# Optimization experiments

Measured on AMD Instinct MI355X. Metric: run time of the kernel, lower is better.

The kernel has to match this reference:

```python
import jax, jax.numpy as jnp
import numpy as np

B = 128
T = 784
H = 256
N_CLASSES = 10


def setup_inputs() -> dict:
    key = jax.random.key(0)
    ks = jax.random.split(key, 7)
    s = 1.0 / np.sqrt(H)
    inputs = jax.random.normal(ks[0], (B, T), dtype=jnp.float32)
    # fixed permutation, matching np.random.RandomState(92916).permutation(784)
    perm = jnp.asarray(np.random.RandomState(92916).permutation(T), dtype=jnp.int32)
    W_ih = jax.random.uniform(ks[1], (4 * H, 1), jnp.float32, -s, s)
    W_hh = jax.random.uniform(ks[2], (4 * H, H), jnp.float32, -s, s)
    b_ih = jax.random.uniform(ks[3], (4 * H,), jnp.float32, -s, s)
    b_hh = jax.random.uniform(ks[4], (4 * H,), jnp.float32, -s, s)
    lin_W = jax.random.uniform(ks[5], (N_CLASSES, H), jnp.float32, -s, s)
    lin_b = jax.random.uniform(ks[6], (N_CLASSES,), jnp.float32, -s, s)
    return {"inputs": inputs, "perm": perm, "W_ih": W_ih, "W_hh": W_hh,
            "b_ih": b_ih, "b_hh": b_hh, "lin_W": lin_W, "lin_b": lin_b}


def reference(inputs, perm, W_ih, W_hh, b_ih, b_hh, lin_W, lin_b):
    # permuted sequential MNIST
    x = inputs[:, perm]                      # [B, T]
    b = b_ih + b_hh                          # [4H]
    w_in = W_ih[:, 0]                        # [4H], input size is 1

    def step(carry, x_t):
        h, c = carry                         # each [B, H]
        gates = x_t[:, None] * w_in[None, :] + h @ W_hh.T + b  # [B, 4H]
        i, f, g, o = jnp.split(gates, 4, axis=-1)
        i = jax.nn.sigmoid(i)
        f = jax.nn.sigmoid(f)
        g = jnp.tanh(g)
        o = jax.nn.sigmoid(o)
        c = f * c + i * g
        h = o * jnp.tanh(c)
        return (h, c), None

    h0 = jnp.zeros((x.shape[0], W_hh.shape[1]), dtype=x.dtype)
    (h, c), _ = jax.lax.scan(step, (h0, h0), x.T)  # scan over T, xs [T, B]
    return h @ lin_W.T + lin_b               # [B, n_classes]
```

## Files before the change

kernel.cpp:

```cpp
#include <hip/hip_runtime.h>

#define TSTEPS 784
#define BATCH  128
#define HID    256
#define WPG    8
#define BG     4
#define NGRP   (BATCH / BG)
#define COLS   32
#define RLOC   128
typedef unsigned long long u64;

__global__ void prep_x(const float* __restrict__ in, const int* __restrict__ perm,
                       float* __restrict__ xp) {
    int b = blockIdx.x;
    for (int t = threadIdx.x; t < TSTEPS; t += blockDim.x)
        xp[b * TSTEPS + t] = in[b * TSTEPS + perm[t]];
}

__global__ void prep_slots(u64* __restrict__ slots) {
    int i = blockIdx.x * blockDim.x + threadIdx.x;
    if (i < BATCH * HID)          slots[i] = 0ull;
    else if (i < 2 * BATCH * HID) slots[i] = 0xFFFFFFFF00000000ull;
}

__global__ __launch_bounds__(1024, 4) void lstm_kernel(
    const float* __restrict__ Whh, const float* __restrict__ Wih,
    const float* __restrict__ bih, const float* __restrict__ bhh,
    const float* __restrict__ xp, u64* __restrict__ slots)
{
    __shared__ float h_lds[BG * HID];
    __shared__ float gate_lds[BG * 132];
    __shared__ float x_lds[BG * TSTEPS];
    __shared__ float c_lds[BG * COLS];
    __shared__ float bias_lds[RLOC];
    __shared__ float win_lds[RLOC];

    const int tid = threadIdx.x;
    const int g       = blockIdx.x & 31;
    const int wgi     = blockIdx.x >> 5;
    const int B0      = g * BG;
    const int colbase = wgi * COLS;

    const int r = tid >> 3;
    const int s = tid & 7;
    const int gate = r >> 5;
    const int R = gate * 256 + colbase + (r & 31);

    float4 w0, w1, w2, w3, w4, w5, w6, w7;
    {
        const float4* wp = (const float4*)(Whh + R * HID + s * 32);
        w0 = wp[(0 + s) & 7]; w1 = wp[(1 + s) & 7];
        w2 = wp[(2 + s) & 7]; w3 = wp[(3 + s) & 7];
        w4 = wp[(4 + s) & 7]; w5 = wp[(5 + s) & 7];
        w6 = wp[(6 + s) & 7]; w7 = wp[(7 + s) & 7];
    }
    #define KEEP4(V) asm volatile("" : "+v"((V).x), "+v"((V).y), "+v"((V).z), "+v"((V).w))
    KEEP4(w0); KEEP4(w1); KEEP4(w2); KEEP4(w3);
    KEEP4(w4); KEEP4(w5); KEEP4(w6); KEEP4(w7);
    #undef KEEP4

    if (tid < RLOC) {
        int gr = (tid >> 5) * 256 + colbase + (tid & 31);
        bias_lds[tid] = bih[gr] + bhh[gr];
        win_lds[tid]  = Wih[gr];
    }
    #pragma unroll
    for (int b = 0; b < BG; ++b)
        if (tid < TSTEPS) x_lds[b * TSTEPS + tid] = xp[(B0 + b) * TSTEPS + tid];
    if (tid < BG * COLS) c_lds[tid] = 0.f;
    __syncthreads();

    const int pb = tid >> 8, pk = tid & 255;
    u64* const slot0 = slots + (B0 + pb) * HID + pk;
    u64* const slot1 = slots + BATCH * HID + (B0 + pb) * HID + pk;

    for (int t = 0; t < TSTEPS; ++t) {
        {
            u64* sp = (t & 1) ? slot1 : slot0;
            u64 v;
            do {
                v = __hip_atomic_load(sp, __ATOMIC_RELAXED, __HIP_MEMORY_SCOPE_AGENT);
            } while ((unsigned)(v >> 32) != (unsigned)t);
            h_lds[tid] = __uint_as_float((unsigned)v);
        }
        __syncthreads();

        float a0 = 0.f, a1 = 0.f, a2 = 0.f, a3 = 0.f;
        const float* hbase = h_lds + s * 32;
        #define DOT_STEP(d, wd)                                              \
        {                                                                    \
            int off = (((d) + s) & 7) * 4;                                   \
            float4 hq0 = *(const float4*)(hbase + off);                      \
            float4 hq1 = *(const float4*)(hbase + 256 + off);                \
            float4 hq2 = *(const float4*)(hbase + 512 + off);                \
            float4 hq3 = *(const float4*)(hbase + 768 + off);                \
            a0 = fmaf(wd.x, hq0.x, a0); a0 = fmaf(wd.y, hq0.y, a0);          \
            a0 = fmaf(wd.z, hq0.z, a0); a0 = fmaf(wd.w, hq0.w, a0);          \
            a1 = fmaf(wd.x, hq1.x, a1); a1 = fmaf(wd.y, hq1.y, a1);          \
            a1 = fmaf(wd.z, hq1.z, a1); a1 = fmaf(wd.w, hq1.w, a1);          \
            a2 = fmaf(wd.x, hq2.x, a2); a2 = fmaf(wd.y, hq2.y, a2);          \
            a2 = fmaf(wd.z, hq2.z, a2); a2 = fmaf(wd.w, hq2.w, a2);          \
            a3 = fmaf(wd.x, hq3.x, a3); a3 = fmaf(wd.y, hq3.y, a3);          \
            a3 = fmaf(wd.z, hq3.z, a3); a3 = fmaf(wd.w, hq3.w, a3);          \
        }
        DOT_STEP(0, w0) DOT_STEP(1, w1) DOT_STEP(2, w2) DOT_STEP(3, w3)
        DOT_STEP(4, w4) DOT_STEP(5, w5) DOT_STEP(6, w6) DOT_STEP(7, w7)
        #undef DOT_STEP

        #pragma unroll
        for (int m = 1; m < 8; m <<= 1) {
            a0 += __shfl_xor(a0, m, 64);
            a1 += __shfl_xor(a1, m, 64);
            a2 += __shfl_xor(a2, m, 64);
            a3 += __shfl_xor(a3, m, 64);
        }
        if (s < BG) {
            float sum = (s == 0) ? a0 : (s == 1) ? a1 : (s == 2) ? a2 : a3;
            float xv = x_lds[s * TSTEPS + t];
            float full = fmaf(win_lds[r], xv, sum + bias_lds[r]);
            float act;
            if (gate == 2) act = 2.f / (1.f + __expf(-2.f * full)) - 1.f;
            else           act = 1.f / (1.f + __expf(-full));
            gate_lds[s * 132 + r] = act;
        }
        __syncthreads();

        if (tid < BG * COLS) {
            int b = tid >> 5, j = tid & 31;
            float iv = gate_lds[b * 132 + j];
            float fv = gate_lds[b * 132 + 32 + j];
            float gv = gate_lds[b * 132 + 64 + j];
            float ov = gate_lds[b * 132 + 96 + j];
            float cn = fmaf(fv, c_lds[tid], iv * gv);
            c_lds[tid] = cn;
            float tc = 2.f / (1.f + __expf(-2.f * cn)) - 1.f;
            float hn = ov * tc;
            u64 val = ((u64)(unsigned)(t + 1) << 32) | (u64)__float_as_uint(hn);
            u64* dp = slots + ((t + 1) & 1) * (BATCH * HID)
                            + (B0 + b) * HID + colbase + j;
            __hip_atomic_store(dp, val, __ATOMIC_RELAXED, __HIP_MEMORY_SCOPE_AGENT);
        }
    }
}

__global__ void out_kernel(const u64* __restrict__ slots, const float* __restrict__ linW,
                           const float* __restrict__ linb, float* __restrict__ out) {
    __shared__ float hl[HID];
    int b = blockIdx.x;
    for (int k = threadIdx.x; k < HID; k += blockDim.x)
        hl[k] = __uint_as_float((unsigned)slots[b * HID + k]);
    __syncthreads();
    if (threadIdx.x < 10) {
        int n = threadIdx.x;
        float acc = linb[n];
        for (int k = 0; k < HID; ++k) acc = fmaf(hl[k], linW[n * HID + k], acc);
        out[b * 10 + n] = acc;
    }
}

extern "C" void kernel_launch(void* const* d_in, const int* in_sizes, int n_in,
                              void* d_out, int out_size, void* d_ws, size_t ws_size,
                              hipStream_t stream) {
    const float* inputs = (const float*)d_in[0];
    const int*   perm   = (const int*)d_in[1];
    const float* Wih    = (const float*)d_in[2];
    const float* Whh    = (const float*)d_in[3];
    const float* bih    = (const float*)d_in[4];
    const float* bhh    = (const float*)d_in[5];
    const float* linW   = (const float*)d_in[6];
    const float* linb   = (const float*)d_in[7];
    float* out = (float*)d_out;

    u64*   slots = (u64*)d_ws;
    float* xp    = (float*)(slots + 2 * BATCH * HID);

    prep_x<<<BATCH, 256, 0, stream>>>(inputs, perm, xp);
    prep_slots<<<(2 * BATCH * HID + 255) / 256, 256, 0, stream>>>(slots);
    lstm_kernel<<<NGRP * WPG, 1024, 0, stream>>>(Whh, Wih, bih, bhh, xp, slots);
    out_kernel<<<BATCH, 64, 0, stream>>>(slots, linW, linb, out);
}
```

Baseline: 2.244 ms.

## Restructure LSTM step so each lane owns all four gates, dropping gate LDS barrier

Each 16-lane group now holds the weights of all four gates for one hidden column and computes two batch rows, so the whole cell update (gates, c, h) is done in registers and the gate_lds staging and second __syncthreads per step go away. The dot products use packed v_pk_fma_f32 and the cross-lane reduction uses DPP adds instead of shfl_xor. h is double-buffered in padded LDS, which makes one barrier per step enough. The trade-off is redundant activation math across the 16 lanes and hand-written inline asm whose correctness depends on DPP row semantics.

```diff
diff --git a/kernel.cpp b/kernel.cpp
--- a/kernel.cpp
+++ b/kernel.cpp
@@ -7,8 +7,11 @@
 #define BG     4
 #define NGRP   (BATCH / BG)
 #define COLS   32
-#define RLOC   128
+#define KSTR   68
+#define HBUF   (16 * KSTR)
 typedef unsigned long long u64;
+typedef float v4f __attribute__((ext_vector_type(4)));
+typedef float v2f __attribute__((ext_vector_type(2)));
 
 __global__ void prep_x(const float* __restrict__ in, const int* __restrict__ perm,
                        float* __restrict__ xp) {
@@ -23,17 +26,22 @@
     else if (i < 2 * BATCH * HID) slots[i] = 0xFFFFFFFF00000000ull;
 }
 
+#define PK_FMA(acc, a, b) \
+    asm("v_pk_fma_f32 %0, %1, %2, %0" : "+v"(acc) : "v"(a), "v"(b))
+#define DPP_ADD(x, ctl) asm("v_add_f32 %0, %1, %0 " ctl " row_mask:0xf bank_mask:0xf" \
+                            : "+v"(x) : "v"(x))
+#define LO2(V) __builtin_shufflevector(V, V, 0, 1)
+#define HI2(V) __builtin_shufflevector(V, V, 2, 3)
+
 __global__ __launch_bounds__(1024, 4) void lstm_kernel(
     const float* __restrict__ Whh, const float* __restrict__ Wih,
     const float* __restrict__ bih, const float* __restrict__ bhh,
     const float* __restrict__ xp, u64* __restrict__ slots)
 {
-    __shared__ float h_lds[BG * HID];
-    __shared__ float gate_lds[BG * 132];
+    __shared__ float h_lds[2][HBUF];
     __shared__ float x_lds[BG * TSTEPS];
-    __shared__ float c_lds[BG * COLS];
-    __shared__ float bias_lds[RLOC];
-    __shared__ float win_lds[RLOC];
+    __shared__ v4f   bias4[COLS];
+    __shared__ v4f   win4[COLS];
 
     const int tid = threadIdx.x;
     const int g       = blockIdx.x & 31;
@@ -41,104 +49,155 @@
     const int B0      = g * BG;
     const int colbase = wgi * COLS;
 
-    const int r = tid >> 3;
-    const int s = tid & 7;
-    const int gate = r >> 5;
-    const int R = gate * 256 + colbase + (r & 31);
-
-    float4 w0, w1, w2, w3, w4, w5, w6, w7;
-    {
-        const float4* wp = (const float4*)(Whh + R * HID + s * 32);
-        w0 = wp[(0 + s) & 7]; w1 = wp[(1 + s) & 7];
-        w2 = wp[(2 + s) & 7]; w3 = wp[(3 + s) & 7];
-        w4 = wp[(4 + s) & 7]; w5 = wp[(5 + s) & 7];
-        w6 = wp[(6 + s) & 7]; w7 = wp[(7 + s) & 7];
-    }
-    #define KEEP4(V) asm volatile("" : "+v"((V).x), "+v"((V).y), "+v"((V).z), "+v"((V).w))
-    KEEP4(w0); KEEP4(w1); KEEP4(w2); KEEP4(w3);
-    KEEP4(w4); KEEP4(w5); KEEP4(w6); KEEP4(w7);
-    #undef KEEP4
-
-    if (tid < RLOC) {
-        int gr = (tid >> 5) * 256 + colbase + (tid & 31);
-        bias_lds[tid] = bih[gr] + bhh[gr];
-        win_lds[tid]  = Wih[gr];
-    }
+    const int ks  = tid & 15;
+    const int bp  = (tid >> 4) & 1;
+    const int col = tid >> 5;
+
+    v4f w[4][4];
     #pragma unroll
-    for (int b = 0; b < BG; ++b)
-        if (tid < TSTEPS) x_lds[b * TSTEPS + tid] = xp[(B0 + b) * TSTEPS + tid];
-    if (tid < BG * COLS) c_lds[tid] = 0.f;
+    for (int q = 0; q < 4; ++q) {
+        const v4f* wp = (const v4f*)(Whh + (q * 256 + colbase + col) * HID + 16 * ks);
+        w[q][0] = wp[0]; w[q][1] = wp[1]; w[q][2] = wp[2]; w[q][3] = wp[3];
+    }
+    if (tid < COLS) {
+        v4f b4, w4_;
+        #pragma unroll
+        for (int q = 0; q < 4; ++q) {
+            int R = q * 256 + colbase + tid;
+            b4[q] = bih[R] + bhh[R];
+            w4_[q] = Wih[R];
+        }
+        bias4[tid] = b4; win4[tid] = w4_;
+    }
+    #pragma unroll
+    for (int bb = 0; bb < BG; ++bb)
+        if (tid < TSTEPS) x_lds[bb * TSTEPS + tid] = xp[(B0 + bb) * TSTEPS + tid];
     __syncthreads();
 
     const int pb = tid >> 8, pk = tid & 255;
     u64* const slot0 = slots + (B0 + pb) * HID + pk;
     u64* const slot1 = slots + BATCH * HID + (B0 + pb) * HID + pk;
+    const int hidx = (pk >> 4) * KSTR + pb * 16 + (pk & 15);
+
+    float c0 = 0.f, c1 = 0.f;
 
     for (int t = 0; t < TSTEPS; ++t) {
-        {
-            u64* sp = (t & 1) ? slot1 : slot0;
+        const int cur = t & 1;
+        #pragma unroll
+        for (int q = 0; q < 4; ++q)
+            asm volatile("" : "+v"(w[q][0]), "+v"(w[q][1]), "+v"(w[q][2]), "+v"(w[q][3]));
+
+        {
+            u64* sp = cur ? slot1 : slot0;
             u64 v;
-            do {
-                v = __hip_atomic_load(sp, __ATOMIC_RELAXED, __HIP_MEMORY_SCOPE_AGENT);
+            do { v = __hip_atomic_load(sp, __ATOMIC_RELAXED, __HIP_MEMORY_SCOPE_AGENT);
             } while ((unsigned)(v >> 32) != (unsigned)t);
-            h_lds[tid] = __uint_as_float((unsigned)v);
+            h_lds[cur][hidx] = __uint_as_float((unsigned)v);
         }
         __syncthreads();
 
-        float a0 = 0.f, a1 = 0.f, a2 = 0.f, a3 = 0.f;
-        const float* hbase = h_lds + s * 32;
-        #define DOT_STEP(d, wd)                                              \
-        {                                                                    \
-            int off = (((d) + s) & 7) * 4;                                   \
-            float4 hq0 = *(const float4*)(hbase + off);                      \
-            float4 hq1 = *(const float4*)(hbase + 256 + off);                \
-            float4 hq2 = *(const float4*)(hbase + 512 + off);                \
-            float4 hq3 = *(const float4*)(hbase + 768 + off);                \
-            a0 = fmaf(wd.x, hq0.x, a0); a0 = fmaf(wd.y, hq0.y, a0);          \
-            a0 = fmaf(wd.z, hq0.z, a0); a0 = fmaf(wd.w, hq0.w, a0);          \
-            a1 = fmaf(wd.x, hq1.x, a1); a1 = fmaf(wd.y, hq1.y, a1);          \
-            a1 = fmaf(wd.z, hq1.z, a1); a1 = fmaf(wd.w, hq1.w, a1);          \
-            a2 = fmaf(wd.x, hq2.x, a2); a2 = fmaf(wd.y, hq2.y, a2);          \
-            a2 = fmaf(wd.z, hq2.z, a2); a2 = fmaf(wd.w, hq2.w, a2);          \
-            a3 = fmaf(wd.x, hq3.x, a3); a3 = fmaf(wd.y, hq3.y, a3);          \
-            a3 = fmaf(wd.z, hq3.z, a3); a3 = fmaf(wd.w, hq3.w, a3);          \
-        }
-        DOT_STEP(0, w0) DOT_STEP(1, w1) DOT_STEP(2, w2) DOT_STEP(3, w3)
-        DOT_STEP(4, w4) DOT_STEP(5, w5) DOT_STEP(6, w6) DOT_STEP(7, w7)
-        #undef DOT_STEP
-
-        #pragma unroll
-        for (int m = 1; m < 8; m <<= 1) {
-            a0 += __shfl_xor(a0, m, 64);
-            a1 += __shfl_xor(a1, m, 64);
-            a2 += __shfl_xor(a2, m, 64);
-            a3 += __shfl_xor(a3, m, 64);
-        }
-        if (s < BG) {
-            float sum = (s == 0) ? a0 : (s == 1) ? a1 : (s == 2) ? a2 : a3;
-            float xv = x_lds[s * TSTEPS + t];
-            float full = fmaf(win_lds[r], xv, sum + bias_lds[r]);
-            float act;
-            if (gate == 2) act = 2.f / (1.f + __expf(-2.f * full)) - 1.f;
-            else           act = 1.f / (1.f + __expf(-full));
-            gate_lds[s * 132 + r] = act;
-        }
-        __syncthreads();
-
-        if (tid < BG * COLS) {
-            int b = tid >> 5, j = tid & 31;
-            float iv = gate_lds[b * 132 + j];
-            float fv = gate_lds[b * 132 + 32 + j];
-            float gv = gate_lds[b * 132 + 64 + j];
-            float ov = gate_lds[b * 132 + 96 + j];
-            float cn = fmaf(fv, c_lds[tid], iv * gv);
-            c_lds[tid] = cn;
-            float tc = 2.f / (1.f + __expf(-2.f * cn)) - 1.f;
-            float hn = ov * tc;
-            u64 val = ((u64)(unsigned)(t + 1) << 32) | (u64)__float_as_uint(hn);
-            u64* dp = slots + ((t + 1) & 1) * (BATCH * HID)
-                            + (B0 + b) * HID + colbase + j;
-            __hip_atomic_store(dp, val, __ATOMIC_RELAXED, __HIP_MEMORY_SCOPE_AGENT);
+        const float* hb = &h_lds[cur][ks * KSTR + bp * 32];
+        v2f a00 = {0.f,0.f}, a10 = {0.f,0.f}, a20 = {0.f,0.f}, a30 = {0.f,0.f};
+        v2f a01 = {0.f,0.f}, a11 = {0.f,0.f}, a21 = {0.f,0.f}, a31 = {0.f,0.f};
+        {
+            v4f hc0 = *(const v4f*)(hb + 0);
+            v4f hc1 = *(const v4f*)(hb + 4);
+            v4f hc2 = *(const v4f*)(hb + 8);
+            v4f hc3 = *(const v4f*)(hb + 12);
+            PK_FMA(a00, LO2(w[0][0]), LO2(hc0)); PK_FMA(a00, HI2(w[0][0]), HI2(hc0));
+            PK_FMA(a00, LO2(w[0][1]), LO2(hc1)); PK_FMA(a00, HI2(w[0][1]), HI2(hc1));
+            PK_FMA(a00, LO2(w[0][2]), LO2(hc2)); PK_FMA(a00, HI2(w[0][2]), HI2(hc2));
+            PK_FMA(a00, LO2(w[0][3]), LO2(hc3)); PK_FMA(a00, HI2(w[0][3]), HI2(hc3));
+            PK_FMA(a10, LO2(w[1][0]), LO2(hc0)); PK_FMA(a10, HI2(w[1][0]), HI2(hc0));
+            PK_FMA(a10, LO2(w[1][1]), LO2(hc1)); PK_FMA(a10, HI2(w[1][1]), HI2(hc1));
+            PK_FMA(a10, LO2(w[1][2]), LO2(hc2)); PK_FMA(a10, HI2(w[1][2]), HI2(hc2));
+            PK_FMA(a10, LO2(w[1][3]), LO2(hc3)); PK_FMA(a10, HI2(w[1][3]), HI2(hc3));
+            PK_FMA(a20, LO2(w[2][0]), LO2(hc0)); PK_FMA(a20, HI2(w[2][0]), HI2(hc0));
+            PK_FMA(a20, LO2(w[2][1]), LO2(hc1)); PK_FMA(a20, HI2(w[2][1]), HI2(hc1));
+            PK_FMA(a20, LO2(w[2][2]), LO2(hc2)); PK_FMA(a20, HI2(w[2][2]), HI2(hc2));
+            PK_FMA(a20, LO2(w[2][3]), LO2(hc3)); PK_FMA(a20, HI2(w[2][3]), HI2(hc3));
+            PK_FMA(a30, LO2(w[3][0]), LO2(hc0)); PK_FMA(a30, HI2(w[3][0]), HI2(hc0));
+            PK_FMA(a30, LO2(w[3][1]), LO2(hc1)); PK_FMA(a30, HI2(w[3][1]), HI2(hc1));
+            PK_FMA(a30, LO2(w[3][2]), LO2(hc2)); PK_FMA(a30, HI2(w[3][2]), HI2(hc2));
+            PK_FMA(a30, LO2(w[3][3]), LO2(hc3)); PK_FMA(a30, HI2(w[3][3]), HI2(hc3));
+        }
+        {
+            v4f hc0 = *(const v4f*)(hb + 16);
+            v4f hc1 = *(const v4f*)(hb + 20);
+            v4f hc2 = *(const v4f*)(hb + 24);
+            v4f hc3 = *(const v4f*)(hb + 28);
+            PK_FMA(a01, LO2(w[0][0]), LO2(hc0)); PK_FMA(a01, HI2(w[0][0]), HI2(hc0));
+            PK_FMA(a01, LO2(w[0][1]), LO2(hc1)); PK_FMA(a01, HI2(w[0][1]), HI2(hc1));
+            PK_FMA(a01, LO2(w[0][2]), LO2(hc2)); PK_FMA(a01, HI2(w[0][2]), HI2(hc2));
+            PK_FMA(a01, LO2(w[0][3]), LO2(hc3)); PK_FMA(a01, HI2(w[0][3]), HI2(hc3));
+            PK_FMA(a11, LO2(w[1][0]), LO2(hc0)); PK_FMA(a11, HI2(w[1][0]), HI2(hc0));
+            PK_FMA(a11, LO2(w[1][1]), LO2(hc1)); PK_FMA(a11, HI2(w[1][1]), HI2(hc1));
+            PK_FMA(a11, LO2(w[1][2]), LO2(hc2)); PK_FMA(a11, HI2(w[1][2]), HI2(hc2));
+            PK_FMA(a11, LO2(w[1][3]), LO2(hc3)); PK_FMA(a11, HI2(w[1][3]), HI2(hc3));
+            PK_FMA(a21, LO2(w[2][0]), LO2(hc0)); PK_FMA(a21, HI2(w[2][0]), HI2(hc0));
+            PK_FMA(a21, LO2(w[2][1]), LO2(hc1)); PK_FMA(a21, HI2(w[2][1]), HI2(hc1));
+            PK_FMA(a21, LO2(w[2][2]), LO2(hc2)); PK_FMA(a21, HI2(w[2][2]), HI2(hc2));
+            PK_FMA(a21, LO2(w[2][3]), LO2(hc3)); PK_FMA(a21, HI2(w[2][3]), HI2(hc3));
+            PK_FMA(a31, LO2(w[3][0]), LO2(hc0)); PK_FMA(a31, HI2(w[3][0]), HI2(hc0));
+            PK_FMA(a31, LO2(w[3][1]), LO2(hc1)); PK_FMA(a31, HI2(w[3][1]), HI2(hc1));
+            PK_FMA(a31, LO2(w[3][2]), LO2(hc2)); PK_FMA(a31, HI2(w[3][2]), HI2(hc2));
+            PK_FMA(a31, LO2(w[3][3]), LO2(hc3)); PK_FMA(a31, HI2(w[3][3]), HI2(hc3));
+        }
+        float s00 = a00.x + a00.y, s10 = a10.x + a10.y;
+        float s20 = a20.x + a20.y, s30 = a30.x + a30.y;
+        float s01 = a01.x + a01.y, s11 = a11.x + a11.y;
+        float s21 = a21.x + a21.y, s31 = a31.x + a31.y;
+
+        #define RSTAGE(ctl) \
+            DPP_ADD(s00, ctl); DPP_ADD(s10, ctl); DPP_ADD(s20, ctl); DPP_ADD(s30, ctl); \
+            DPP_ADD(s01, ctl); DPP_ADD(s11, ctl); DPP_ADD(s21, ctl); DPP_ADD(s31, ctl);
+        RSTAGE("quad_perm:[1,0,3,2]")
+        RSTAGE("quad_perm:[2,3,0,1]")
+        RSTAGE("row_half_mirror")
+        RSTAGE("row_mirror")
+        #undef RSTAGE
+
+        v4f b4 = bias4[col];
+        v4f wn = win4[col];
+        {
+            float xv = x_lds[(2 * bp) * TSTEPS + t];
+            float p0 = fmaf(wn.x, xv, s00 + b4.x);
+            float p1 = fmaf(wn.y, xv, s10 + b4.y);
+            float p2 = fmaf(wn.z, xv, s20 + b4.z);
+            float p3 = fmaf(wn.w, xv, s30 + b4.w);
+            float iv = 1.f / (1.f + __expf(-p0));
+            float fv = 1.f / (1.f + __expf(-p1));
+            float gv = 2.f / (1.f + __expf(-2.f * p2)) - 1.f;
+            float ov = 1.f / (1.f + __expf(-p3));
+            c0 = fmaf(fv, c0, iv * gv);
+            float th = 2.f / (1.f + __expf(-2.f * c0)) - 1.f;
+            float hn = ov * th;
+            if (ks == 0) {
+                u64 val = ((u64)(unsigned)(t + 1) << 32) | (u64)__float_as_uint(hn);
+                u64* dp = slots + ((t + 1) & 1) * (BATCH * HID)
+                                + (B0 + 2 * bp) * HID + colbase + col;
+                __hip_atomic_store(dp, val, __ATOMIC_RELAXED, __HIP_MEMORY_SCOPE_AGENT);
+            }
+        }
+        {
+            float xv = x_lds[(2 * bp + 1) * TSTEPS + t];
+            float p0 = fmaf(wn.x, xv, s01 + b4.x);
+            float p1 = fmaf(wn.y, xv, s11 + b4.y);
+            float p2 = fmaf(wn.z, xv, s21 + b4.z);
+            float p3 = fmaf(wn.w, xv, s31 + b4.w);
+            float iv = 1.f / (1.f + __expf(-p0));
+            float fv = 1.f / (1.f + __expf(-p1));
+            float gv = 2.f / (1.f + __expf(-2.f * p2)) - 1.f;
+            float ov = 1.f / (1.f + __expf(-p3));
+            c1 = fmaf(fv, c1, iv * gv);
+            float th = 2.f / (1.f + __expf(-2.f * c1)) - 1.f;
+            float hn = ov * th;
+            if (ks == 0) {
+                u64 val = ((u64)(unsigned)(t + 1) << 32) | (u64)__float_as_uint(hn);
+                u64* dp = slots + ((t + 1) & 1) * (BATCH * HID)
+                                + (B0 + 2 * bp + 1) * HID + colbase + col;
+                __hip_atomic_store(dp, val, __ATOMIC_RELAXED, __HIP_MEMORY_SCOPE_AGENT);
+            }
         }
     }
 }
```

New measurement: 3.337 ms. 1.49x slower.
